# Kernel optimization log

Measured on AMD Instinct MI355X. Metric: run time of the kernel, lower is better.

Reference implementation:

```python
import jax, jax.numpy as jnp
import numpy as np

TEMP = 13.544
EPS = 1e-5  # BatchNorm2d default eps


def setup_inputs() -> dict:
    key = jax.random.key(0)
    k1, = jax.random.split(key, 1)
    N, S, E = 16, 1024, 512
    x = jax.random.normal(k1, (N, S, E), dtype=jnp.float32)
    gamma = jnp.ones((1,), dtype=jnp.float32)   # BatchNorm2d(1).weight
    beta = jnp.zeros((1,), dtype=jnp.float32)   # BatchNorm2d(1).bias
    return {"x": x, "gamma": gamma, "beta": beta}


def reference(x, gamma, beta):
    # Pairwise squared L2 distances via GEMM identity:
    # ||a-b||^2 = ||a||^2 + ||b||^2 - 2 a.b   (symmetric, matches the
    # original broadcast diff+square+sum without the O(S^2 E) intermediate)
    sq = jnp.sum(x * x, axis=-1)                    # (N, S)
    gram = jnp.einsum('bse,bte->bst', x, x)         # (N, S, S)
    d = sq[:, :, None] + sq[:, None, :] - 2.0 * gram  # (N, S, S)
    d = jnp.maximum(d, 0.0)                          # numerical floor (exact math is >= 0)

    # BatchNorm2d(1) in training mode: stats over all elements of the single channel
    d = d[:, None, :, :]                             # (N, 1, S, S)
    mean = jnp.mean(d)
    var = jnp.mean((d - mean) ** 2)                  # biased variance, as torch uses for normalization
    d_hat = (d - mean) * jax.lax.rsqrt(var + EPS)
    out = d_hat * gamma.reshape(1, 1, 1, 1) + beta.reshape(1, 1, 1, 1)

    # softmax(-out / 13.544) over last dim
    return jax.nn.softmax(-out / TEMP, axis=-1)      # (N, 1, S, S)
```

## Files before the change

kernel.cpp:

```cpp
#include <hip/hip_runtime.h>
#include <hip/hip_bf16.h>


#define S_DIM 1024
#define E_DIM 512
#define NBATCH 16
#define TEMP_C 13.544

typedef __attribute__((ext_vector_type(4))) float f32x4;
typedef __attribute__((ext_vector_type(8))) short bf16x8;

__device__ inline unsigned pkbf(float lo, float hi) {
  unsigned a = __float_as_uint(lo), b = __float_as_uint(hi);
  a = (a + 0x7FFFu + ((a >> 16) & 1u)) >> 16;
  b = (b + 0x7FFFu + ((b >> 16) & 1u)) & 0xFFFF0000u;
  return b | a;
}

__device__ inline void gload16(const void* g, void* l) {
  __builtin_amdgcn_global_load_lds(
      (const __attribute__((address_space(1))) unsigned*)g,
      (__attribute__((address_space(3))) unsigned*)l, 16, 0, 0);
}

__global__ __launch_bounds__(256) void sqcvt(const float* __restrict__ x,
                                             ushort* __restrict__ xb16,
                                             float* __restrict__ sq,
                                             double* __restrict__ sums) {
  const int wave = threadIdx.x >> 6, lane = threadIdx.x & 63;
  const size_t row = (size_t)blockIdx.x * 4 + wave;
  const float4* xr = reinterpret_cast<const float4*>(x + row * E_DIM);
  float4 a = xr[lane * 2], b = xr[lane * 2 + 1];
  uint4 p;
  p.x = pkbf(a.x, a.y); p.y = pkbf(a.z, a.w);
  p.z = pkbf(b.x, b.y); p.w = pkbf(b.z, b.w);
  *reinterpret_cast<uint4*>(xb16 + row * E_DIM + lane * 8) = p;
  float s = a.x*a.x + a.y*a.y + a.z*a.z + a.w*a.w +
            b.x*b.x + b.y*b.y + b.z*b.z + b.w*b.w;
#pragma unroll
  for (int o = 32; o > 0; o >>= 1) s += __shfl_xor(s, o);
  if (lane == 0) sq[row] = s;
  if (blockIdx.x == 0 && threadIdx.x == 0) { sums[0] = 0.0; sums[1] = 0.0; }
}

__global__ __launch_bounds__(256) void gram2(const ushort* __restrict__ xb16,
                                             const float* __restrict__ sq,
                                             float* __restrict__ dout,
                                             double* __restrict__ sums) {
  __shared__ ushort lA[128 * 32];
  __shared__ ushort lB[128 * 32];
  __shared__ double red[8];

  const int tid = threadIdx.x, wave = tid >> 6, lane = tid & 63;
  const int wr = wave >> 1, wc = wave & 1;

  const int bid = blockIdx.x;
  const int xcd = bid & 7, li = bid >> 3;
  const int b = (xcd << 1) | (li >> 6);
  const int tile = li & 63;
  const int tr = tile >> 3, tc = tile & 7;

  const ushort* xb = xb16 + (size_t)b * (S_DIM * E_DIM);
  const int rowA0 = tr * 128, rowB0 = tc * 128;

  int eA[2], eB[2];
  const int o0 = wave * 1024 + lane * 16;
#pragma unroll
  for (int i = 0; i < 2; ++i) {
    int o = o0 + i * 4096;
    int so = o ^ (((o >> 7) & 3) << 4);
    int row = so >> 6, cb = (so >> 4) & 3;
    eA[i] = (rowA0 + row) * E_DIM + cb * 8;
    eB[i] = (rowB0 + row) * E_DIM + cb * 8;
  }

  f32x4 acc[4][4] = {};

#pragma unroll 1
  for (int ks = 0; ks < E_DIM / 32; ++ks) {
    const int k0 = ks * 32;
    gload16(xb + eA[0] + k0, (char*)lA + wave * 1024);
    gload16(xb + eA[1] + k0, (char*)lA + 4096 + wave * 1024);
    gload16(xb + eB[0] + k0, (char*)lB + wave * 1024);
    gload16(xb + eB[1] + k0, (char*)lB + 4096 + wave * 1024);
    __syncthreads();
    bf16x8 af[4], bfr[4];
    const int cb = lane >> 4;
#pragma unroll
    for (int m = 0; m < 4; ++m) {
      int row = wr * 64 + m * 16 + (lane & 15);
      af[m] = *reinterpret_cast<const bf16x8*>(
          (const char*)lA + row * 64 + ((cb ^ ((row >> 1) & 3)) << 4));
    }
#pragma unroll
    for (int n = 0; n < 4; ++n) {
      int row = wc * 64 + n * 16 + (lane & 15);
      bfr[n] = *reinterpret_cast<const bf16x8*>(
          (const char*)lB + row * 64 + ((cb ^ ((row >> 1) & 3)) << 4));
    }
#pragma unroll
    for (int m = 0; m < 4; ++m)
#pragma unroll
      for (int n = 0; n < 4; ++n)
        acc[m][n] = __builtin_amdgcn_mfma_f32_16x16x32_bf16(af[m], bfr[n], acc[m][n], 0, 0, 0);
    __syncthreads();
  }

  const float* sqb = sq + b * S_DIM;
  float* dbase = dout + (size_t)b * S_DIM * S_DIM;
  double sd = 0.0, sd2 = 0.0;
#pragma unroll
  for (int m = 0; m < 4; ++m) {
    int gr0 = tr * 128 + wr * 64 + m * 16 + ((lane >> 4) << 2);
    float sqr0 = sqb[gr0], sqr1 = sqb[gr0 + 1], sqr2 = sqb[gr0 + 2], sqr3 = sqb[gr0 + 3];
#pragma unroll
    for (int n = 0; n < 4; ++n) {
      int gc = tc * 128 + wc * 64 + n * 16 + (lane & 15);
      float sqc = sqb[gc];
      float d0 = fmaxf(sqr0 + sqc - 2.0f * acc[m][n][0], 0.0f);
      float d1 = fmaxf(sqr1 + sqc - 2.0f * acc[m][n][1], 0.0f);
      float d2 = fmaxf(sqr2 + sqc - 2.0f * acc[m][n][2], 0.0f);
      float d3 = fmaxf(sqr3 + sqc - 2.0f * acc[m][n][3], 0.0f);
      dbase[(size_t)(gr0 + 0) * S_DIM + gc] = d0;
      dbase[(size_t)(gr0 + 1) * S_DIM + gc] = d1;
      dbase[(size_t)(gr0 + 2) * S_DIM + gc] = d2;
      dbase[(size_t)(gr0 + 3) * S_DIM + gc] = d3;
      sd += (double)d0 + (double)d1 + (double)d2 + (double)d3;
      sd2 += (double)d0 * d0 + (double)d1 * d1 + (double)d2 * d2 + (double)d3 * d3;
    }
  }
#pragma unroll
  for (int o = 32; o > 0; o >>= 1) {
    sd += __shfl_xor(sd, o);
    sd2 += __shfl_xor(sd2, o);
  }
  if (lane == 0) { red[wave] = sd; red[4 + wave] = sd2; }
  __syncthreads();
  if (tid == 0) {
    atomicAdd(&sums[0], red[0] + red[1] + red[2] + red[3]);
    atomicAdd(&sums[1], red[4] + red[5] + red[6] + red[7]);
  }
}

__global__ __launch_bounds__(256) void sq_kernel(const float* __restrict__ x,
                                                 float* __restrict__ sq,
                                                 double* __restrict__ sums) {
  int row = blockIdx.x * 4 + (threadIdx.x >> 6);
  int lane = threadIdx.x & 63;
  const float4* xr = reinterpret_cast<const float4*>(x + (size_t)row * E_DIM);
  float4 a = xr[lane], b = xr[lane + 64];
  float s = a.x*a.x + a.y*a.y + a.z*a.z + a.w*a.w +
            b.x*b.x + b.y*b.y + b.z*b.z + b.w*b.w;
#pragma unroll
  for (int o = 32; o > 0; o >>= 1) s += __shfl_xor(s, o);
  if (lane == 0) sq[row] = s;
  if (blockIdx.x == 0 && threadIdx.x == 0) { sums[0] = 0.0; sums[1] = 0.0; }
}

__global__ __launch_bounds__(256, 2) void gram_fb(const float* __restrict__ x,
                                                  const float* __restrict__ sq,
                                                  float* __restrict__ dout,
                                                  double* __restrict__ sums) {
  __shared__ short ldsA[2][128][32];
  __shared__ short ldsB[2][128][32];
  __shared__ double red[8];
  const int b = blockIdx.x >> 6;
  const int tile = blockIdx.x & 63;
  const int tr = tile >> 3, tc = tile & 7;
  const int tid = threadIdx.x;
  const int wave = tid >> 6, lane = tid & 63;
  const int wr = wave >> 1, wc = wave & 1;
  const float* xb = x + (size_t)b * S_DIM * E_DIM;
  const int rowA0 = tr * 128, rowB0 = tc * 128;
  f32x4 acc[4][4] = {};
  auto stage = [&](int buf, int k0) {
#pragma unroll
    for (int i = 0; i < 4; ++i) {
      int c = tid + 256 * i;
      int row = c >> 3;
      int c4 = (c & 7) * 4;
      float4 va = *reinterpret_cast<const float4*>(xb + (size_t)(rowA0 + row) * E_DIM + k0 + c4);
      float4 vb = *reinterpret_cast<const float4*>(xb + (size_t)(rowB0 + row) * E_DIM + k0 + c4);
      *reinterpret_cast<uint2*>(&ldsA[buf][row][c4]) = make_uint2(pkbf(va.x, va.y), pkbf(va.z, va.w));
      *reinterpret_cast<uint2*>(&ldsB[buf][row][c4]) = make_uint2(pkbf(vb.x, vb.y), pkbf(vb.z, vb.w));
    }
  };
  stage(0, 0);
  __syncthreads();
  int buf = 0;
#pragma unroll 1
  for (int ks = 0; ks < E_DIM / 32; ++ks) {
    bf16x8 af[4], bfr[4];
#pragma unroll
    for (int m = 0; m < 4; ++m)
      af[m] = *reinterpret_cast<const bf16x8*>(&ldsA[buf][wr*64 + m*16 + (lane&15)][(lane>>4)*8]);
#pragma unroll
    for (int n = 0; n < 4; ++n)
      bfr[n] = *reinterpret_cast<const bf16x8*>(&ldsB[buf][wc*64 + n*16 + (lane&15)][(lane>>4)*8]);
    if (ks + 1 < E_DIM / 32) stage(buf ^ 1, (ks + 1) * 32);
#pragma unroll
    for (int m = 0; m < 4; ++m)
#pragma unroll
      for (int n = 0; n < 4; ++n)
        acc[m][n] = __builtin_amdgcn_mfma_f32_16x16x32_bf16(af[m], bfr[n], acc[m][n], 0, 0, 0);
    __syncthreads();
    buf ^= 1;
  }
  const float* sqb = sq + b * S_DIM;
  float* dbase = dout + (size_t)b * S_DIM * S_DIM;
  double sd = 0.0, sd2 = 0.0;
#pragma unroll
  for (int m = 0; m < 4; ++m) {
    int gr0 = tr * 128 + wr * 64 + m * 16 + ((lane >> 4) << 2);
    float sqr0 = sqb[gr0], sqr1 = sqb[gr0+1], sqr2 = sqb[gr0+2], sqr3 = sqb[gr0+3];
#pragma unroll
    for (int n = 0; n < 4; ++n) {
      int gc = tc * 128 + wc * 64 + n * 16 + (lane & 15);
      float sqc = sqb[gc];
      float d0 = fmaxf(sqr0 + sqc - 2.0f * acc[m][n][0], 0.0f);
      float d1 = fmaxf(sqr1 + sqc - 2.0f * acc[m][n][1], 0.0f);
      float d2 = fmaxf(sqr2 + sqc - 2.0f * acc[m][n][2], 0.0f);
      float d3 = fmaxf(sqr3 + sqc - 2.0f * acc[m][n][3], 0.0f);
      dbase[(size_t)(gr0+0)*S_DIM + gc] = d0;
      dbase[(size_t)(gr0+1)*S_DIM + gc] = d1;
      dbase[(size_t)(gr0+2)*S_DIM + gc] = d2;
      dbase[(size_t)(gr0+3)*S_DIM + gc] = d3;
      sd += (double)d0 + (double)d1 + (double)d2 + (double)d3;
      sd2 += (double)d0*d0 + (double)d1*d1 + (double)d2*d2 + (double)d3*d3;
    }
  }
#pragma unroll
  for (int o = 32; o > 0; o >>= 1) { sd += __shfl_xor(sd, o); sd2 += __shfl_xor(sd2, o); }
  if (lane == 0) { red[wave] = sd; red[4 + wave] = sd2; }
  __syncthreads();
  if (tid == 0) {
    atomicAdd(&sums[0], red[0] + red[1] + red[2] + red[3]);
    atomicAdd(&sums[1], red[4] + red[5] + red[6] + red[7]);
  }
}

__global__ __launch_bounds__(256) void softmax2(float* __restrict__ d,
                                                const double* __restrict__ sums,
                                                const float* __restrict__ gamma) {
  const int wave = threadIdx.x >> 6, lane = threadIdx.x & 63;
  const size_t row = (size_t)blockIdx.x * 4 + wave;
  constexpr double invN = 1.0 / (16.0 * 1024.0 * 1024.0);
  double mean = sums[0] * invN;
  double var = sums[1] * invN - mean * mean;
  float scale = (float)(-((double)gamma[0]) / (sqrt(var + 1e-5) * TEMP_C));

  float4* r4 = reinterpret_cast<float4*>(d + row * S_DIM);
  float4 v[4];
#pragma unroll
  for (int i = 0; i < 4; ++i) v[i] = r4[lane + 64 * i];
  float l[16];
#pragma unroll
  for (int i = 0; i < 4; ++i) {
    l[4*i+0] = scale * v[i].x; l[4*i+1] = scale * v[i].y;
    l[4*i+2] = scale * v[i].z; l[4*i+3] = scale * v[i].w;
  }
  float mx = l[0];
#pragma unroll
  for (int i = 1; i < 16; ++i) mx = fmaxf(mx, l[i]);
#pragma unroll
  for (int o = 32; o > 0; o >>= 1) mx = fmaxf(mx, __shfl_xor(mx, o));
  const float L2E = 1.4426950408889634f;
  float e[16], s = 0.f;
#pragma unroll
  for (int i = 0; i < 16; ++i) { e[i] = exp2f((l[i] - mx) * L2E); s += e[i]; }
#pragma unroll
  for (int o = 32; o > 0; o >>= 1) s += __shfl_xor(s, o);
  float inv = 1.0f / s;
#pragma unroll
  for (int i = 0; i < 4; ++i)
    r4[lane + 64 * i] = make_float4(e[4*i]*inv, e[4*i+1]*inv, e[4*i+2]*inv, e[4*i+3]*inv);
}

extern "C" void kernel_launch(void* const* d_in, const int* in_sizes, int n_in,
                              void* d_out, int out_size, void* d_ws, size_t ws_size,
                              hipStream_t stream) {
  const float* x = (const float*)d_in[0];
  const float* gamma = (const float*)d_in[1];
  float* out = (float*)d_out;
  double* sums = (double*)d_ws;
  float* sq = (float*)((char*)d_ws + 256);
  ushort* xb16 = (ushort*)((char*)d_ws + 256 + 65536);
  const size_t need = 256 + 65536 + (size_t)NBATCH * S_DIM * E_DIM * 2;

  if (ws_size >= need) {
    sqcvt<<<dim3(NBATCH * S_DIM / 4), dim3(256), 0, stream>>>(x, xb16, sq, sums);
    gram2<<<dim3(NBATCH * 64), dim3(256), 0, stream>>>(xb16, sq, out, sums);
  } else {
    sq_kernel<<<dim3(NBATCH * S_DIM / 4), dim3(256), 0, stream>>>(x, sq, sums);
    gram_fb<<<dim3(NBATCH * 64), dim3(256), 0, stream>>>(x, sq, out, sums);
  }
  softmax2<<<dim3(NBATCH * S_DIM / 4), dim3(256), 0, stream>>>(out, sums, gamma);
}
```

Measured before the change: 157.2 us.

## Store row-shifted distances as fp16 intermediate and double-buffer GEMM LDS staging

The gram kernel now writes distances minus the row's squared norm as fp16 into a workspace buffer, and a new softmax kernel reads that half-width intermediate and writes fp32 output. Subtracting the row constant is allowed because softmax is shift-invariant per row. The GEMM loop also double-buffers its LDS tiles so the next K-slice's global-to-LDS load is issued before the current slice's MFMAs. The old fp32-input fallback path is removed, so the sqcvt bf16 workspace is now always assumed. This cuts intermediate write and read traffic roughly in half, at the cost of fp16 rounding of the logits and a larger workspace requirement.

```diff
diff --git a/kernel.cpp b/kernel.cpp
--- a/kernel.cpp
+++ b/kernel.cpp
@@ -9,6 +9,7 @@
 
 typedef __attribute__((ext_vector_type(4))) float f32x4;
 typedef __attribute__((ext_vector_type(8))) short bf16x8;
+typedef __attribute__((ext_vector_type(8))) _Float16 f16x8;
 
 __device__ inline unsigned pkbf(float lo, float hi) {
   unsigned a = __float_as_uint(lo), b = __float_as_uint(hi);
@@ -43,12 +44,14 @@
   if (blockIdx.x == 0 && threadIdx.x == 0) { sums[0] = 0.0; sums[1] = 0.0; }
 }
 
-__global__ __launch_bounds__(256) void gram2(const ushort* __restrict__ xb16,
+template <int MODE>
+__global__ __launch_bounds__(256) void gram3(const ushort* __restrict__ xb16,
                                              const float* __restrict__ sq,
                                              float* __restrict__ dout,
+                                             _Float16* __restrict__ dp,
                                              double* __restrict__ sums) {
-  __shared__ ushort lA[128 * 32];
-  __shared__ ushort lB[128 * 32];
+  __shared__ ushort lA[2][4096];
+  __shared__ ushort lB[2][4096];
   __shared__ double red[8];
 
   const int tid = threadIdx.x, wave = tid >> 6, lane = tid & 63;
@@ -74,29 +77,36 @@
     eB[i] = (rowB0 + row) * E_DIM + cb * 8;
   }
 
+  auto stage = [&](int buf, int k0) {
+    char* la = (char*)&lA[buf][0];
+    char* lb = (char*)&lB[buf][0];
+    gload16(xb + eA[0] + k0, la + wave * 1024);
+    gload16(xb + eA[1] + k0, la + 4096 + wave * 1024);
+    gload16(xb + eB[0] + k0, lb + wave * 1024);
+    gload16(xb + eB[1] + k0, lb + 4096 + wave * 1024);
+  };
+
   f32x4 acc[4][4] = {};
 
+  stage(0, 0);
+  __syncthreads();
+  int buf = 0;
 #pragma unroll 1
   for (int ks = 0; ks < E_DIM / 32; ++ks) {
-    const int k0 = ks * 32;
-    gload16(xb + eA[0] + k0, (char*)lA + wave * 1024);
-    gload16(xb + eA[1] + k0, (char*)lA + 4096 + wave * 1024);
-    gload16(xb + eB[0] + k0, (char*)lB + wave * 1024);
-    gload16(xb + eB[1] + k0, (char*)lB + 4096 + wave * 1024);
-    __syncthreads();
+    if (ks + 1 < E_DIM / 32) stage(buf ^ 1, (ks + 1) * 32);
     bf16x8 af[4], bfr[4];
     const int cb = lane >> 4;
+    const char* la = (const char*)&lA[buf][0];
+    const char* lb = (const char*)&lB[buf][0];
 #pragma unroll
     for (int m = 0; m < 4; ++m) {
       int row = wr * 64 + m * 16 + (lane & 15);
-      af[m] = *reinterpret_cast<const bf16x8*>(
-          (const char*)lA + row * 64 + ((cb ^ ((row >> 1) & 3)) << 4));
+      af[m] = *reinterpret_cast<const bf16x8*>(la + row * 64 + ((cb ^ ((row >> 1) & 3)) << 4));
     }
 #pragma unroll
     for (int n = 0; n < 4; ++n) {
       int row = wc * 64 + n * 16 + (lane & 15);
-      bfr[n] = *reinterpret_cast<const bf16x8*>(
-          (const char*)lB + row * 64 + ((cb ^ ((row >> 1) & 3)) << 4));
+      bfr[n] = *reinterpret_cast<const bf16x8*>(lb + row * 64 + ((cb ^ ((row >> 1) & 3)) << 4));
     }
 #pragma unroll
     for (int m = 0; m < 4; ++m)
@@ -104,10 +114,10 @@
       for (int n = 0; n < 4; ++n)
         acc[m][n] = __builtin_amdgcn_mfma_f32_16x16x32_bf16(af[m], bfr[n], acc[m][n], 0, 0, 0);
     __syncthreads();
+    buf ^= 1;
   }
 
   const float* sqb = sq + b * S_DIM;
-  float* dbase = dout + (size_t)b * S_DIM * S_DIM;
   double sd = 0.0, sd2 = 0.0;
 #pragma unroll
   for (int m = 0; m < 4; ++m) {
@@ -121,10 +131,19 @@
       float d1 = fmaxf(sqr1 + sqc - 2.0f * acc[m][n][1], 0.0f);
       float d2 = fmaxf(sqr2 + sqc - 2.0f * acc[m][n][2], 0.0f);
       float d3 = fmaxf(sqr3 + sqc - 2.0f * acc[m][n][3], 0.0f);
-      dbase[(size_t)(gr0 + 0) * S_DIM + gc] = d0;
-      dbase[(size_t)(gr0 + 1) * S_DIM + gc] = d1;
-      dbase[(size_t)(gr0 + 2) * S_DIM + gc] = d2;
-      dbase[(size_t)(gr0 + 3) * S_DIM + gc] = d3;
+      if (MODE == 0) {
+        float* dbase = dout + (size_t)b * S_DIM * S_DIM;
+        dbase[(size_t)(gr0 + 0) * S_DIM + gc] = d0;
+        dbase[(size_t)(gr0 + 1) * S_DIM + gc] = d1;
+        dbase[(size_t)(gr0 + 2) * S_DIM + gc] = d2;
+        dbase[(size_t)(gr0 + 3) * S_DIM + gc] = d3;
+      } else {
+        _Float16* dbase = dp + (size_t)b * S_DIM * S_DIM;
+        dbase[(size_t)(gr0 + 0) * S_DIM + gc] = (_Float16)(d0 - sqr0);
+        dbase[(size_t)(gr0 + 1) * S_DIM + gc] = (_Float16)(d1 - sqr1);
+        dbase[(size_t)(gr0 + 2) * S_DIM + gc] = (_Float16)(d2 - sqr2);
+        dbase[(size_t)(gr0 + 3) * S_DIM + gc] = (_Float16)(d3 - sqr3);
+      }
       sd += (double)d0 + (double)d1 + (double)d2 + (double)d3;
       sd2 += (double)d0 * d0 + (double)d1 * d1 + (double)d2 * d2 + (double)d3 * d3;
     }
@@ -142,113 +161,19 @@
   }
 }
 
-__global__ __launch_bounds__(256) void sq_kernel(const float* __restrict__ x,
-                                                 float* __restrict__ sq,
-                                                 double* __restrict__ sums) {
-  int row = blockIdx.x * 4 + (threadIdx.x >> 6);
-  int lane = threadIdx.x & 63;
-  const float4* xr = reinterpret_cast<const float4*>(x + (size_t)row * E_DIM);
-  float4 a = xr[lane], b = xr[lane + 64];
-  float s = a.x*a.x + a.y*a.y + a.z*a.z + a.w*a.w +
-            b.x*b.x + b.y*b.y + b.z*b.z + b.w*b.w;
-#pragma unroll
-  for (int o = 32; o > 0; o >>= 1) s += __shfl_xor(s, o);
-  if (lane == 0) sq[row] = s;
-  if (blockIdx.x == 0 && threadIdx.x == 0) { sums[0] = 0.0; sums[1] = 0.0; }
-}
-
-__global__ __launch_bounds__(256, 2) void gram_fb(const float* __restrict__ x,
-                                                  const float* __restrict__ sq,
-                                                  float* __restrict__ dout,
-                                                  double* __restrict__ sums) {
-  __shared__ short ldsA[2][128][32];
-  __shared__ short ldsB[2][128][32];
-  __shared__ double red[8];
-  const int b = blockIdx.x >> 6;
-  const int tile = blockIdx.x & 63;
-  const int tr = tile >> 3, tc = tile & 7;
-  const int tid = threadIdx.x;
-  const int wave = tid >> 6, lane = tid & 63;
-  const int wr = wave >> 1, wc = wave & 1;
-  const float* xb = x + (size_t)b * S_DIM * E_DIM;
-  const int rowA0 = tr * 128, rowB0 = tc * 128;
-  f32x4 acc[4][4] = {};
-  auto stage = [&](int buf, int k0) {
-#pragma unroll
-    for (int i = 0; i < 4; ++i) {
-      int c = tid + 256 * i;
-      int row = c >> 3;
-      int c4 = (c & 7) * 4;
-      float4 va = *reinterpret_cast<const float4*>(xb + (size_t)(rowA0 + row) * E_DIM + k0 + c4);
-      float4 vb = *reinterpret_cast<const float4*>(xb + (size_t)(rowB0 + row) * E_DIM + k0 + c4);
-      *reinterpret_cast<uint2*>(&ldsA[buf][row][c4]) = make_uint2(pkbf(va.x, va.y), pkbf(va.z, va.w));
-      *reinterpret_cast<uint2*>(&ldsB[buf][row][c4]) = make_uint2(pkbf(vb.x, vb.y), pkbf(vb.z, vb.w));
-    }
-  };
-  stage(0, 0);
-  __syncthreads();
-  int buf = 0;
-#pragma unroll 1
-  for (int ks = 0; ks < E_DIM / 32; ++ks) {
-    bf16x8 af[4], bfr[4];
-#pragma unroll
-    for (int m = 0; m < 4; ++m)
-      af[m] = *reinterpret_cast<const bf16x8*>(&ldsA[buf][wr*64 + m*16 + (lane&15)][(lane>>4)*8]);
-#pragma unroll
-    for (int n = 0; n < 4; ++n)
-      bfr[n] = *reinterpret_cast<const bf16x8*>(&ldsB[buf][wc*64 + n*16 + (lane&15)][(lane>>4)*8]);
-    if (ks + 1 < E_DIM / 32) stage(buf ^ 1, (ks + 1) * 32);
-#pragma unroll
-    for (int m = 0; m < 4; ++m)
-#pragma unroll
-      for (int n = 0; n < 4; ++n)
-        acc[m][n] = __builtin_amdgcn_mfma_f32_16x16x32_bf16(af[m], bfr[n], acc[m][n], 0, 0, 0);
-    __syncthreads();
-    buf ^= 1;
-  }
-  const float* sqb = sq + b * S_DIM;
-  float* dbase = dout + (size_t)b * S_DIM * S_DIM;
-  double sd = 0.0, sd2 = 0.0;
-#pragma unroll
-  for (int m = 0; m < 4; ++m) {
-    int gr0 = tr * 128 + wr * 64 + m * 16 + ((lane >> 4) << 2);
-    float sqr0 = sqb[gr0], sqr1 = sqb[gr0+1], sqr2 = sqb[gr0+2], sqr3 = sqb[gr0+3];
-#pragma unroll
-    for (int n = 0; n < 4; ++n) {
-      int gc = tc * 128 + wc * 64 + n * 16 + (lane & 15);
-      float sqc = sqb[gc];
-      float d0 = fmaxf(sqr0 + sqc - 2.0f * acc[m][n][0], 0.0f);
-      float d1 = fmaxf(sqr1 + sqc - 2.0f * acc[m][n][1], 0.0f);
-      float d2 = fmaxf(sqr2 + sqc - 2.0f * acc[m][n][2], 0.0f);
-      float d3 = fmaxf(sqr3 + sqc - 2.0f * acc[m][n][3], 0.0f);
-      dbase[(size_t)(gr0+0)*S_DIM + gc] = d0;
-      dbase[(size_t)(gr0+1)*S_DIM + gc] = d1;
-      dbase[(size_t)(gr0+2)*S_DIM + gc] = d2;
-      dbase[(size_t)(gr0+3)*S_DIM + gc] = d3;
-      sd += (double)d0 + (double)d1 + (double)d2 + (double)d3;
-      sd2 += (double)d0*d0 + (double)d1*d1 + (double)d2*d2 + (double)d3*d3;
-    }
-  }
-#pragma unroll
-  for (int o = 32; o > 0; o >>= 1) { sd += __shfl_xor(sd, o); sd2 += __shfl_xor(sd2, o); }
-  if (lane == 0) { red[wave] = sd; red[4 + wave] = sd2; }
-  __syncthreads();
-  if (tid == 0) {
-    atomicAdd(&sums[0], red[0] + red[1] + red[2] + red[3]);
-    atomicAdd(&sums[1], red[4] + red[5] + red[6] + red[7]);
-  }
-}
-
-__global__ __launch_bounds__(256) void softmax2(float* __restrict__ d,
-                                                const double* __restrict__ sums,
-                                                const float* __restrict__ gamma) {
-  const int wave = threadIdx.x >> 6, lane = threadIdx.x & 63;
-  const size_t row = (size_t)blockIdx.x * 4 + wave;
+__device__ inline float ln_scale(const double* sums, const float* gamma) {
   constexpr double invN = 1.0 / (16.0 * 1024.0 * 1024.0);
   double mean = sums[0] * invN;
   double var = sums[1] * invN - mean * mean;
-  float scale = (float)(-((double)gamma[0]) / (sqrt(var + 1e-5) * TEMP_C));
-
+  return (float)(-((double)gamma[0]) / (sqrt(var + 1e-5) * TEMP_C));
+}
+
+__global__ __launch_bounds__(256) void softmax_f32(float* __restrict__ d,
+                                                   const double* __restrict__ sums,
+                                                   const float* __restrict__ gamma) {
+  const int wave = threadIdx.x >> 6, lane = threadIdx.x & 63;
+  const size_t row = (size_t)blockIdx.x * 4 + wave;
+  const float scale = ln_scale(sums, gamma);
   float4* r4 = reinterpret_cast<float4*>(d + row * S_DIM);
   float4 v[4];
 #pragma unroll
@@ -274,6 +199,36 @@
 #pragma unroll
   for (int i = 0; i < 4; ++i)
     r4[lane + 64 * i] = make_float4(e[4*i]*inv, e[4*i+1]*inv, e[4*i+2]*inv, e[4*i+3]*inv);
+}
+
+__global__ __launch_bounds__(256) void softmax_f16(const _Float16* __restrict__ dp,
+                                                   float* __restrict__ out,
+                                                   const double* __restrict__ sums,
+                                                   const float* __restrict__ gamma) {
+  const int wave = threadIdx.x >> 6, lane = threadIdx.x & 63;
+  const size_t row = (size_t)blockIdx.x * 4 + wave;
+  const float scale = ln_scale(sums, gamma);
+  const f16x8* r8 = reinterpret_cast<const f16x8*>(dp + row * S_DIM);
+  f16x8 h0 = r8[lane * 2], h1 = r8[lane * 2 + 1];
+  float l[16];
+#pragma unroll
+  for (int i = 0; i < 8; ++i) { l[i] = scale * (float)h0[i]; l[8 + i] = scale * (float)h1[i]; }
+  float mx = l[0];
+#pragma unroll
+  for (int i = 1; i < 16; ++i) mx = fmaxf(mx, l[i]);
+#pragma unroll
+  for (int o = 32; o > 0; o >>= 1) mx = fmaxf(mx, __shfl_xor(mx, o));
+  const float L2E = 1.4426950408889634f;
+  float e[16], s = 0.f;
+#pragma unroll
+  for (int i = 0; i < 16; ++i) { e[i] = exp2f((l[i] - mx) * L2E); s += e[i]; }
+#pragma unroll
+  for (int o = 32; o > 0; o >>= 1) s += __shfl_xor(s, o);
+  float inv = 1.0f / s;
+  float4* o4 = reinterpret_cast<float4*>(out + row * S_DIM);
+#pragma unroll
+  for (int i = 0; i < 4; ++i)
+    o4[lane * 4 + i] = make_float4(e[4*i]*inv, e[4*i+1]*inv, e[4*i+2]*inv, e[4*i+3]*inv);
 }
 
 extern "C" void kernel_launch(void* const* d_in, const int* in_sizes, int n_in,
@@ -285,14 +240,17 @@
   double* sums = (double*)d_ws;
   float* sq = (float*)((char*)d_ws + 256);
   ushort* xb16 = (ushort*)((char*)d_ws + 256 + 65536);
-  const size_t need = 256 + 65536 + (size_t)NBATCH * S_DIM * E_DIM * 2;
-
-  if (ws_size >= need) {
-    sqcvt<<<dim3(NBATCH * S_DIM / 4), dim3(256), 0, stream>>>(x, xb16, sq, sums);
-    gram2<<<dim3(NBATCH * 64), dim3(256), 0, stream>>>(xb16, sq, out, sums);
+  _Float16* dp = (_Float16*)((char*)d_ws + 256 + 65536 +
+                             (size_t)NBATCH * S_DIM * E_DIM * 2);
+  const size_t need_b = 256 + 65536 + (size_t)NBATCH * S_DIM * E_DIM * 2;
+  const size_t need_a = need_b + (size_t)NBATCH * S_DIM * S_DIM * 2;
+
+  sqcvt<<<dim3(NBATCH * S_DIM / 4), dim3(256), 0, stream>>>(x, xb16, sq, sums);
+  if (ws_size >= need_a) {
+    gram3<1><<<dim3(NBATCH * 64), dim3(256), 0, stream>>>(xb16, sq, out, dp, sums);
+    softmax_f16<<<dim3(NBATCH * S_DIM / 4), dim3(256), 0, stream>>>(dp, out, sums, gamma);
   } else {
-    sq_kernel<<<dim3(NBATCH * S_DIM / 4), dim3(256), 0, stream>>>(x, sq, sums);
-    gram_fb<<<dim3(NBATCH * 64), dim3(256), 0, stream>>>(x, sq, out, sums);
-  }
-  softmax2<<<dim3(NBATCH * S_DIM / 4), dim3(256), 0, stream>>>(out, sums, gamma);
-}
+    gram3<0><<<dim3(NBATCH * 64), dim3(256), 0, stream>>>(xb16, sq, out, dp, sums);
+    softmax_f32<<<dim3(NBATCH * S_DIM / 4), dim3(256), 0, stream>>>(out, sums, gamma);
+  }
+}
```

Result: no change. 158.8 us (+1.0%).
